# Performance work log

Hardware: AMD Instinct MI355X
Metric: run time of the kernel (lower is better)

## Reference

```python
import jax, jax.numpy as jnp
import numpy as np

N = 50000
E = 800000
D_IN, D_HID, D_OUT = 128, 128, 64


def setup_inputs() -> dict:
    key = jax.random.key(0)
    ks = jax.random.split(key, 8)
    x = jax.random.normal(ks[0], (N, D_IN), dtype=jnp.float32)
    edge_index = jax.random.randint(ks[1], (2, E), 0, N, dtype=jnp.int64)
    # Glorot-ish init for GCNConv linear weights + zero bias (PyG default bias=True)
    def lin(k, din, dout):
        s = 1.0 / np.sqrt(din)
        return jax.random.uniform(k, (din, dout), jnp.float32, -s, s)
    return {
        "x": x,
        "edge_index": edge_index,
        "W1": lin(ks[2], D_IN, D_HID), "b1": jnp.zeros((D_HID,), jnp.float32),
        "W2": lin(ks[3], D_HID, D_HID), "b2": jnp.zeros((D_HID,), jnp.float32),
        "W3": lin(ks[4], D_HID, D_OUT), "b3": jnp.zeros((D_OUT,), jnp.float32),
    }


def _prep_edges(edge_index, n):
    # add self loops (PyG GCNConv default add_self_loops=True)
    loop = jnp.arange(n, dtype=edge_index.dtype)
    src = jnp.concatenate([edge_index[0], loop])
    dst = jnp.concatenate([edge_index[1], loop])
    deg = jax.ops.segment_sum(jnp.ones_like(dst, dtype=jnp.float32), dst, num_segments=n)
    dinv = jnp.where(deg > 0, jax.lax.rsqrt(deg), 0.0)
    norm = dinv[src] * dinv[dst]  # symmetric normalization per edge
    return src, dst, norm


def _gcn_conv(h, W, b, src, dst, norm, n):
    h = h @ W                                   # [N, dout]
    msg = h[src] * norm[:, None]                # [E+N, dout] gather
    out = jax.ops.segment_sum(msg, dst, num_segments=n)  # scatter-add
    return out + b


def reference(x, edge_index, W1, b1, W2, b2, W3, b3):
    src, dst, norm = _prep_edges(edge_index, N)
    h = jax.nn.relu(_gcn_conv(x, W1, b1, src, dst, norm, N))
    h = jax.nn.relu(_gcn_conv(h, W2, b2, src, dst, norm, N))
    return _gcn_conv(h, W3, b3, src, dst, norm, N)  # eval mode: dropout is identity
```

## Files before the change

kernel.cpp:

```cpp
#include <hip/hip_runtime.h>
#include <hip/hip_fp16.h>
#include <math.h>

#define NN 50000
#define NE 800000
#define RAWSTRIDE 96
#define NBUCK 196
#define NBBIN 196
#define BCAP 4608
#define ACH 4096
#define G1B 782

using bf8v = __attribute__((ext_vector_type(8))) short;
using f4v  = __attribute__((ext_vector_type(4))) float;

__device__ inline unsigned short f2bf(float f) {
    unsigned int u = __float_as_uint(f);
    u += 0x7FFFu + ((u >> 16) & 1u);
    return (unsigned short)(u >> 16);
}
__device__ inline float bflo(unsigned int d) { return __uint_as_float(d << 16); }
__device__ inline float bfhi(unsigned int d) { return __uint_as_float(d & 0xFFFF0000u); }


__device__ __forceinline__ void bin_body(const int* __restrict__ src,
                                         const int* __restrict__ dst,
                                         int* __restrict__ gcursor,
                                         unsigned int* __restrict__ bst,
                                         int bx, char* shc) {
    unsigned int* items = (unsigned int*)shc;
    int* cnt    = (int*)(shc + 16384);
    int* pref   = (int*)(shc + 17408);
    int* gstart = (int*)(shc + 18436);
    const int t = threadIdx.x;
    cnt[t] = 0;
    __syncthreads();
    const int base = bx * ACH;

    unsigned int my[16]; int myb[16], myr[16];
    #pragma unroll
    for (int i = 0; i < 16; ++i) {
        int e = base + i * 256 + t;
        my[i] = 0; myb[i] = -1; myr[i] = 0;
        if (e < NE) {
            int d = dst[e], s = src[e];
            my[i] = (unsigned int)s | ((unsigned int)d << 16);
            int b = d >> 8;
            myb[i] = b;
            myr[i] = atomicAdd(&cnt[b], 1);
        }
    }
    __syncthreads();
    if (t == 0) {
        int run = 0;
        for (int b = 0; b < 256; ++b) { pref[b] = run; run += cnt[b]; }
        pref[256] = run;
    }
    __syncthreads();
    if (cnt[t] > 0) gstart[t] = atomicAdd(&gcursor[t], cnt[t]);
    __syncthreads();
    #pragma unroll
    for (int i = 0; i < 16; ++i)
        if (myb[i] >= 0) items[pref[myb[i]] + myr[i]] = my[i];
    __syncthreads();
    const int total = pref[256];
    for (int i = t; i < total; i += 256) {
        int lo = 0, hi = 255;
        while (lo < hi) { int mid = (lo + hi + 1) >> 1; if (pref[mid] <= i) lo = mid; else hi = mid - 1; }
        int idx = gstart[lo] + (i - pref[lo]);
        if (idx < BCAP) bst[(size_t)lo * BCAP + idx] = items[i];
    }
}


__global__ __launch_bounds__(512) void sortb_kernel(const int* __restrict__ gcursor,
                                                    const unsigned int* __restrict__ bst,
                                                    int* __restrict__ cnt_g,
                                                    float* __restrict__ dinv,
                                                    unsigned short* __restrict__ raw) {
    __shared__ unsigned int items[BCAP];
    __shared__ int cnt[256], pref[257], cur[256];
    __shared__ unsigned short outl[BCAP];
    const int b = blockIdx.x;
    const int t = threadIdx.x;
    int n = gcursor[b];
    if (n > BCAP) n = BCAP;
    if (t < 256) { cnt[t] = 0; cur[t] = 0; }
    __syncthreads();
    for (int i = t; i < n; i += 512) {
        unsigned int u = bst[(size_t)b * BCAP + i];
        items[i] = u;
        atomicAdd(&cnt[(u >> 16) & 255], 1);
    }
    __syncthreads();
    if (t == 0) {
        int run = 0;
        for (int j = 0; j < 256; ++j) { pref[j] = run; run += cnt[j]; }
        pref[256] = run;
    }
    __syncthreads();
    for (int i = t; i < n; i += 512) {
        unsigned int u = items[i];
        int ln = (u >> 16) & 255;
        int r = atomicAdd(&cur[ln], 1);
        outl[pref[ln] + r] = (unsigned short)(u & 0xFFFFu);
    }
    __syncthreads();
    for (int i = t; i < n; i += 512) {
        int lo = 0, hi = 255;
        while (lo < hi) { int mid = (lo + hi + 1) >> 1; if (pref[mid] <= i) lo = mid; else hi = mid - 1; }
        int r = i - pref[lo];
        if (r < RAWSTRIDE) raw[(size_t)(b * 256 + lo) * RAWSTRIDE + r] = outl[i];
    }
    if (t < 256) {
        int node = b * 256 + t;
        if (node < NN) {
            int c = cnt[t];
            cnt_g[node] = c;
            dinv[node] = rsqrtf((float)(1 + c));
        }
    }
}


__device__ __forceinline__ void gemm128_body_f32(const float* __restrict__ A,
                                                 const float* __restrict__ W,
                                                 unsigned short* __restrict__ out,
                                                 int bx, char* shc) {
    unsigned short* Wt = (unsigned short*)shc;
    unsigned short* Dt = (unsigned short*)(shc + 128 * 136 * 2);
    const int t = threadIdx.x;
    const int row0 = bx * 64;

    {
        int n = t & 127;
        int kbase = (t >> 7) * 4;
        for (int kk = kbase; kk < 128; kk += 8) {
            float w0 = W[(kk + 0) * 128 + n];
            float w1 = W[(kk + 1) * 128 + n];
            float w2 = W[(kk + 2) * 128 + n];
            float w3 = W[(kk + 3) * 128 + n];
            unsigned int p0 = (unsigned int)f2bf(w0) | ((unsigned int)f2bf(w1) << 16);
            unsigned int p1 = (unsigned int)f2bf(w2) | ((unsigned int)f2bf(w3) << 16);
            *(unsigned int*)&Wt[n * 136 + kk]     = p0;
            *(unsigned int*)&Wt[n * 136 + kk + 2] = p1;
        }
    }
    __syncthreads();

    const int wave = t >> 6;
    const int lane = t & 63;
    const int m16  = lane & 15;
    const int quad = lane >> 4;
    const int arow = row0 + wave * 16 + m16;
    const int arowc = (arow < NN) ? arow : 0;

    f4v acc[8];
    #pragma unroll
    for (int i = 0; i < 8; ++i) acc[i] = (f4v)(0.0f);

    #pragma unroll
    for (int k0 = 0; k0 < 128; k0 += 32) {
        bf8v afrag;
        const float4* ap = (const float4*)(A + (size_t)arowc * 128 + k0 + quad * 8);
        float4 a0 = ap[0], a1 = ap[1];
        afrag[0] = (short)f2bf(a0.x); afrag[1] = (short)f2bf(a0.y);
        afrag[2] = (short)f2bf(a0.z); afrag[3] = (short)f2bf(a0.w);
        afrag[4] = (short)f2bf(a1.x); afrag[5] = (short)f2bf(a1.y);
        afrag[6] = (short)f2bf(a1.z); afrag[7] = (short)f2bf(a1.w);
        #pragma unroll
        for (int nt = 0; nt < 8; ++nt) {
            bf8v bfrag = *(const bf8v*)&Wt[(nt * 16 + m16) * 136 + k0 + quad * 8];
            acc[nt] = __builtin_amdgcn_mfma_f32_16x16x32_bf16(afrag, bfrag, acc[nt], 0, 0, 0);
        }
    }

    #pragma unroll
    for (int nt = 0; nt < 8; ++nt) {
        #pragma unroll
        for (int r = 0; r < 4; ++r) {
            Dt[(wave * 16 + quad * 4 + r) * 136 + nt * 16 + m16] = f2bf(acc[nt][r]);
        }
    }
    __syncthreads();

    {
        int r = t >> 2;
        int c = t & 3;
        int gr = row0 + r;
        if (gr < NN) {
            const uint4* s = (const uint4*)&Dt[r * 136] + c * 4;
            uint4* d = (uint4*)(out + (size_t)gr * 128) + c * 4;
            d[0] = s[0]; d[1] = s[1]; d[2] = s[2]; d[3] = s[3];
        }
    }
}

__global__ __launch_bounds__(256) void bin_g1_kernel(const int* __restrict__ src,
                                                     const int* __restrict__ dst,
                                                     int* __restrict__ gcursor,
                                                     unsigned int* __restrict__ bst,
                                                     const float* __restrict__ x,
                                                     const float* __restrict__ W1,
                                                     unsigned short* __restrict__ hb) {
    __shared__ __align__(16) char sh[52224];
    if (blockIdx.x < NBBIN) {
        bin_body(src, dst, gcursor, bst, blockIdx.x, sh);
    } else {
        gemm128_body_f32(x, W1, hb, blockIdx.x - NBBIN, sh);
    }
}


#define AGG128_BODY(HV, RROW, C, DIW, LANE, ACCV)                                   \
    {                                                                               \
        uint4 g = HV[(size_t)wid * 16 + (LANE)];                                    \
        float ws = (DIW) * (DIW);                                                   \
        ACCV[0] = ws * bflo(g.x); ACCV[1] = ws * bfhi(g.x);                         \
        ACCV[2] = ws * bflo(g.y); ACCV[3] = ws * bfhi(g.y);                         \
        ACCV[4] = ws * bflo(g.z); ACCV[5] = ws * bfhi(g.z);                         \
        ACCV[6] = ws * bflo(g.w); ACCV[7] = ws * bfhi(g.w);                         \
    }                                                                               \
    const int cfull = (C) & ~7;                                                     \
    uint4 q;                                                                        \
    if (cfull > 0) q = *(const uint4*)(RROW);                                       \
    for (int e = 0; e < cfull; e += 8) {                                            \
        uint4 qc = q;                                                               \
        if (e + 8 < cfull) q = *(const uint4*)((RROW) + e + 8);                     \
        int c0 = qc.x & 0xFFFFu, c1 = qc.x >> 16;                                   \
        int c2 = qc.y & 0xFFFFu, c3 = qc.y >> 16;                                   \
        int c4 = qc.z & 0xFFFFu, c5 = qc.z >> 16;                                   \
        int c6 = qc.w & 0xFFFFu, c7 = qc.w >> 16;                                   \
        uint4 g0 = HV[(size_t)c0 * 16 + (LANE)];                                    \
        uint4 g1 = HV[(size_t)c1 * 16 + (LANE)];                                    \
        uint4 g2 = HV[(size_t)c2 * 16 + (LANE)];                                    \
        uint4 g3 = HV[(size_t)c3 * 16 + (LANE)];                                    \
        uint4 g4 = HV[(size_t)c4 * 16 + (LANE)];                                    \
        uint4 g5 = HV[(size_t)c5 * 16 + (LANE)];                                    \
        uint4 g6 = HV[(size_t)c6 * 16 + (LANE)];                                    \
        uint4 g7 = HV[(size_t)c7 * 16 + (LANE)];                                    \
        float w0 = (DIW) * dinv[c0], w1 = (DIW) * dinv[c1];                         \
        float w2 = (DIW) * dinv[c2], w3 = (DIW) * dinv[c3];                         \
        float w4 = (DIW) * dinv[c4], w5 = (DIW) * dinv[c5];                         \
        float w6 = (DIW) * dinv[c6], w7 = (DIW) * dinv[c7];                         \
        ACC8(g0, w0) ACC8(g1, w1) ACC8(g2, w2) ACC8(g3, w3)                         \
        ACC8(g4, w4) ACC8(g5, w5) ACC8(g6, w6) ACC8(g7, w7)                         \
    }                                                                               \
    if ((C) & 7) {                                                                  \
        int e = cfull, rem = (C) - e;                                               \
        uint4 qc = *(const uint4*)((RROW) + e);                                     \
        int c0 = qc.x & 0xFFFFu, c1 = qc.x >> 16;                                   \
        int c2 = qc.y & 0xFFFFu, c3 = qc.y >> 16;                                   \
        int c4 = qc.z & 0xFFFFu, c5 = qc.z >> 16;                                   \
        int c6 = qc.w & 0xFFFFu, c7 = qc.w >> 16;                                   \
        if (rem <= 1) c1 = 0; if (rem <= 2) c2 = 0; if (rem <= 3) c3 = 0;           \
        if (rem <= 4) c4 = 0; if (rem <= 5) c5 = 0; if (rem <= 6) c6 = 0;           \
        c7 = 0;                                                                     \
        float w0 = (DIW) * dinv[c0];                                                \
        float w1 = (rem > 1) ? (DIW) * dinv[c1] : 0.f;                              \
        float w2 = (rem > 2) ? (DIW) * dinv[c2] : 0.f;                              \
        float w3 = (rem > 3) ? (DIW) * dinv[c3] : 0.f;                              \
        float w4 = (rem > 4) ? (DIW) * dinv[c4] : 0.f;                              \
        float w5 = (rem > 5) ? (DIW) * dinv[c5] : 0.f;                              \
        float w6 = (rem > 6) ? (DIW) * dinv[c6] : 0.f;                              \
        float w7 = 0.f;                                                             \
        uint4 g0 = HV[(size_t)c0 * 16 + (LANE)];                                    \
        uint4 g1 = HV[(size_t)c1 * 16 + (LANE)];                                    \
        uint4 g2 = HV[(size_t)c2 * 16 + (LANE)];                                    \
        uint4 g3 = HV[(size_t)c3 * 16 + (LANE)];                                    \
        uint4 g4 = HV[(size_t)c4 * 16 + (LANE)];                                    \
        uint4 g5 = HV[(size_t)c5 * 16 + (LANE)];                                    \
        uint4 g6 = HV[(size_t)c6 * 16 + (LANE)];                                    \
        uint4 g7 = HV[(size_t)c7 * 16 + (LANE)];                                    \
        ACC8(g0, w0) ACC8(g1, w1) ACC8(g2, w2) ACC8(g3, w3)                         \
        ACC8(g4, w4) ACC8(g5, w5) ACC8(g6, w6) ACC8(g7, w7)                         \
    }

#define ACC8(G, W_) \
    acc[0] += W_ * bflo(G.x); acc[1] += W_ * bfhi(G.x); \
    acc[2] += W_ * bflo(G.y); acc[3] += W_ * bfhi(G.y); \
    acc[4] += W_ * bflo(G.z); acc[5] += W_ * bfhi(G.z); \
    acc[6] += W_ * bflo(G.w); acc[7] += W_ * bfhi(G.w);


__global__ __launch_bounds__(256) void aggW2_kernel(const unsigned short* __restrict__ hin,
                                                    const unsigned short* __restrict__ raw,
                                                    const int* __restrict__ cnt_g,
                                                    const float* __restrict__ dinv,
                                                    const float* __restrict__ bias,
                                                    const float* __restrict__ W,
                                                    unsigned short* __restrict__ out) {
    __shared__ unsigned short Wt[128 * 136];
    __shared__ unsigned short Zt[64 * 136];
    const int t = threadIdx.x;
    const int row0 = blockIdx.x * 64;

    {
        int n = t & 127;
        int kbase = (t >> 7) * 4;
        for (int kk = kbase; kk < 128; kk += 8) {
            float w0 = W[(kk + 0) * 128 + n];
            float w1 = W[(kk + 1) * 128 + n];
            float w2 = W[(kk + 2) * 128 + n];
            float w3 = W[(kk + 3) * 128 + n];
            unsigned int p0 = (unsigned int)f2bf(w0) | ((unsigned int)f2bf(w1) << 16);
            unsigned int p1 = (unsigned int)f2bf(w2) | ((unsigned int)f2bf(w3) << 16);
            *(unsigned int*)&Wt[n * 136 + kk]     = p0;
            *(unsigned int*)&Wt[n * 136 + kk + 2] = p1;
        }
    }

    const int group = t >> 4;
    const int lane  = t & 15;
    const uint4* hv = (const uint4*)hin;
    const float4* bp = (const float4*)bias;
    float4 b0 = bp[lane * 2], b1 = bp[lane * 2 + 1];

    for (int r = 0; r < 4; ++r) {
        const int wid = row0 + r * 16 + group;
        uint4 o = make_uint4(0u, 0u, 0u, 0u);
        if (wid < NN) {
            int c = cnt_g[wid];
            if (c > RAWSTRIDE) c = RAWSTRIDE;
            const float diw = dinv[wid];
            const unsigned short* rrow = raw + (size_t)wid * RAWSTRIDE;
            float acc[8];
            AGG128_BODY(hv, rrow, c, diw, lane, acc)
            acc[0] += b0.x; acc[1] += b0.y; acc[2] += b0.z; acc[3] += b0.w;
            acc[4] += b1.x; acc[5] += b1.y; acc[6] += b1.z; acc[7] += b1.w;
            #pragma unroll
            for (int j = 0; j < 8; ++j) acc[j] = fmaxf(acc[j], 0.f);
            o.x = (unsigned int)f2bf(acc[0]) | ((unsigned int)f2bf(acc[1]) << 16);
            o.y = (unsigned int)f2bf(acc[2]) | ((unsigned int)f2bf(acc[3]) << 16);
            o.z = (unsigned int)f2bf(acc[4]) | ((unsigned int)f2bf(acc[5]) << 16);
            o.w = (unsigned int)f2bf(acc[6]) | ((unsigned int)f2bf(acc[7]) << 16);
        }
        *(uint4*)&Zt[(r * 16 + group) * 136 + lane * 8] = o;
    }
    __syncthreads();

    const int wave = t >> 6;
    const int l64  = t & 63;
    const int m16  = l64 & 15;
    const int quad = l64 >> 4;

    f4v acc[8];
    #pragma unroll
    for (int i = 0; i < 8; ++i) acc[i] = (f4v)(0.0f);

    #pragma unroll
    for (int k0 = 0; k0 < 128; k0 += 32) {
        bf8v afrag = *(const bf8v*)&Zt[(wave * 16 + m16) * 136 + k0 + quad * 8];
        #pragma unroll
        for (int nt = 0; nt < 8; ++nt) {
            bf8v bfrag = *(const bf8v*)&Wt[(nt * 16 + m16) * 136 + k0 + quad * 8];
            acc[nt] = __builtin_amdgcn_mfma_f32_16x16x32_bf16(afrag, bfrag, acc[nt], 0, 0, 0);
        }
    }
    __syncthreads();

    #pragma unroll
    for (int nt = 0; nt < 8; ++nt) {
        #pragma unroll
        for (int r = 0; r < 4; ++r) {
            Zt[(wave * 16 + quad * 4 + r) * 136 + nt * 16 + m16] = f2bf(acc[nt][r]);
        }
    }
    __syncthreads();

    {
        int r = t >> 2;
        int c = t & 3;
        int gr = row0 + r;
        if (gr < NN) {
            const uint4* s = (const uint4*)&Zt[r * 136] + c * 4;
            uint4* d = (uint4*)(out + (size_t)gr * 128) + c * 4;
            d[0] = s[0]; d[1] = s[1]; d[2] = s[2]; d[3] = s[3];
        }
    }
}


__global__ __launch_bounds__(256) void aggG3_kernel(const unsigned short* __restrict__ hin,
                                                    const unsigned short* __restrict__ raw,
                                                    const int* __restrict__ cnt_g,
                                                    const float* __restrict__ dinv,
                                                    const float* __restrict__ bias,
                                                    const float* __restrict__ W,
                                                    unsigned short* __restrict__ outh) {
    constexpr int LD = 132;
    __shared__ float Zt[64 * LD];
    const int t = threadIdx.x;
    const int row0 = blockIdx.x * 64;

    const int group = t >> 4;
    const int lane  = t & 15;
    const uint4* hv = (const uint4*)hin;
    const float4* bp = (const float4*)bias;
    float4 b0 = bp[lane * 2], b1 = bp[lane * 2 + 1];

    for (int r = 0; r < 4; ++r) {
        const int wid = row0 + r * 16 + group;
        float acc[8] = {0.f, 0.f, 0.f, 0.f, 0.f, 0.f, 0.f, 0.f};
        if (wid < NN) {
            int c = cnt_g[wid];
            if (c > RAWSTRIDE) c = RAWSTRIDE;
            const float diw = dinv[wid];
            const unsigned short* rrow = raw + (size_t)wid * RAWSTRIDE;
            AGG128_BODY(hv, rrow, c, diw, lane, acc)
            acc[0] += b0.x; acc[1] += b0.y; acc[2] += b0.z; acc[3] += b0.w;
            acc[4] += b1.x; acc[5] += b1.y; acc[6] += b1.z; acc[7] += b1.w;
            #pragma unroll
            for (int j = 0; j < 8; ++j) acc[j] = fmaxf(acc[j], 0.f);
        }
        float4* zr = (float4*)&Zt[(r * 16 + group) * LD + lane * 8];
        zr[0] = make_float4(acc[0], acc[1], acc[2], acc[3]);
        zr[1] = make_float4(acc[4], acc[5], acc[6], acc[7]);
    }
    __syncthreads();

    constexpr int CG = 16;
    constexpr int RPT = 4;
    const int cg = t % CG;
    const int rt = t / CG;
    const float4* Wv = (const float4*)W;
    float4 acc[RPT];
    #pragma unroll
    for (int i = 0; i < RPT; ++i) acc[i] = make_float4(0.f, 0.f, 0.f, 0.f);

    for (int k0 = 0; k0 < 128; k0 += 4) {
        float4 w0 = Wv[(k0 + 0) * CG + cg];
        float4 w1 = Wv[(k0 + 1) * CG + cg];
        float4 w2 = Wv[(k0 + 2) * CG + cg];
        float4 w3 = Wv[(k0 + 3) * CG + cg];
        #pragma unroll
        for (int i = 0; i < RPT; ++i) {
            const float* lr = Zt + (rt * RPT + i) * LD;
            float4 a = ((const float4*)lr)[k0 >> 2];
            acc[i].x += a.x * w0.x + a.y * w1.x + a.z * w2.x + a.w * w3.x;
            acc[i].y += a.x * w0.y + a.y * w1.y + a.z * w2.y + a.w * w3.y;
            acc[i].z += a.x * w0.z + a.y * w1.z + a.z * w2.z + a.w * w3.z;
            acc[i].w += a.x * w0.w + a.y * w1.w + a.z * w2.w + a.w * w3.w;
        }
    }

    #pragma unroll
    for (int i = 0; i < RPT; ++i) {
        int gr = row0 + rt * RPT + i;
        if (gr < NN) {
            uint2 o;
            o.x = (unsigned int)f2bf(acc[i].x) | ((unsigned int)f2bf(acc[i].y) << 16);
            o.y = (unsigned int)f2bf(acc[i].z) | ((unsigned int)f2bf(acc[i].w) << 16);
            ((uint2*)(outh + (size_t)gr * 64))[cg] = o;
        }
    }
}


__global__ __launch_bounds__(256) void agg3_kernel(const unsigned short* __restrict__ hin,
                                                   const unsigned short* __restrict__ raw,
                                                   const int* __restrict__ cnt_g,
                                                   const float* __restrict__ dinv,
                                                   const float* __restrict__ bias,
                                                   float* __restrict__ out) {
    const int t = threadIdx.x;
    const int group = t >> 3;
    const int lane  = t & 7;
    const int wid = blockIdx.x * 32 + group;
    if (wid >= NN) return;

    int c = cnt_g[wid];
    if (c > RAWSTRIDE) c = RAWSTRIDE;
    const float diw = dinv[wid];
    const unsigned short* rrow = raw + (size_t)wid * RAWSTRIDE;
    const uint4* hv = (const uint4*)hin;

    float acc[8];
    {
        uint4 g = hv[(size_t)wid * 8 + lane];
        float ws = diw * diw;
        acc[0] = ws * bflo(g.x); acc[1] = ws * bfhi(g.x);
        acc[2] = ws * bflo(g.y); acc[3] = ws * bfhi(g.y);
        acc[4] = ws * bflo(g.z); acc[5] = ws * bfhi(g.z);
        acc[6] = ws * bflo(g.w); acc[7] = ws * bfhi(g.w);
    }

    const int cfull = c & ~7;
    uint4 q;
    if (cfull > 0) q = *(const uint4*)(rrow);
    for (int e = 0; e < cfull; e += 8) {
        uint4 qc = q;
        if (e + 8 < cfull) q = *(const uint4*)(rrow + e + 8);
        int c0 = qc.x & 0xFFFFu, c1 = qc.x >> 16;
        int c2 = qc.y & 0xFFFFu, c3 = qc.y >> 16;
        int c4 = qc.z & 0xFFFFu, c5 = qc.z >> 16;
        int c6 = qc.w & 0xFFFFu, c7 = qc.w >> 16;
        uint4 g0 = hv[(size_t)c0 * 8 + lane];
        uint4 g1 = hv[(size_t)c1 * 8 + lane];
        uint4 g2 = hv[(size_t)c2 * 8 + lane];
        uint4 g3 = hv[(size_t)c3 * 8 + lane];
        uint4 g4 = hv[(size_t)c4 * 8 + lane];
        uint4 g5 = hv[(size_t)c5 * 8 + lane];
        uint4 g6 = hv[(size_t)c6 * 8 + lane];
        uint4 g7 = hv[(size_t)c7 * 8 + lane];
        float w0 = diw * dinv[c0], w1 = diw * dinv[c1];
        float w2 = diw * dinv[c2], w3 = diw * dinv[c3];
        float w4 = diw * dinv[c4], w5 = diw * dinv[c5];
        float w6 = diw * dinv[c6], w7 = diw * dinv[c7];
        ACC8(g0, w0) ACC8(g1, w1) ACC8(g2, w2) ACC8(g3, w3)
        ACC8(g4, w4) ACC8(g5, w5) ACC8(g6, w6) ACC8(g7, w7)
    }
    if (c & 7) {
        int e = cfull, rem = c - e;
        uint4 qc = *(const uint4*)(rrow + e);
        int c0 = qc.x & 0xFFFFu, c1 = qc.x >> 16;
        int c2 = qc.y & 0xFFFFu, c3 = qc.y >> 16;
        int c4 = qc.z & 0xFFFFu, c5 = qc.z >> 16;
        int c6 = qc.w & 0xFFFFu, c7 = qc.w >> 16;
        if (rem <= 1) c1 = 0; if (rem <= 2) c2 = 0; if (rem <= 3) c3 = 0;
        if (rem <= 4) c4 = 0; if (rem <= 5) c5 = 0; if (rem <= 6) c6 = 0;
        c7 = 0;
        float w0 = diw * dinv[c0];
        float w1 = (rem > 1) ? diw * dinv[c1] : 0.f;
        float w2 = (rem > 2) ? diw * dinv[c2] : 0.f;
        float w3 = (rem > 3) ? diw * dinv[c3] : 0.f;
        float w4 = (rem > 4) ? diw * dinv[c4] : 0.f;
        float w5 = (rem > 5) ? diw * dinv[c5] : 0.f;
        float w6 = (rem > 6) ? diw * dinv[c6] : 0.f;
        float w7 = 0.f;
        uint4 g0 = hv[(size_t)c0 * 8 + lane];
        uint4 g1 = hv[(size_t)c1 * 8 + lane];
        uint4 g2 = hv[(size_t)c2 * 8 + lane];
        uint4 g3 = hv[(size_t)c3 * 8 + lane];
        uint4 g4 = hv[(size_t)c4 * 8 + lane];
        uint4 g5 = hv[(size_t)c5 * 8 + lane];
        uint4 g6 = hv[(size_t)c6 * 8 + lane];
        uint4 g7 = hv[(size_t)c7 * 8 + lane];
        ACC8(g0, w0) ACC8(g1, w1) ACC8(g2, w2) ACC8(g3, w3)
        ACC8(g4, w4) ACC8(g5, w5) ACC8(g6, w6) ACC8(g7, w7)
    }

    const float4* bp = (const float4*)bias;
    float4 b0 = bp[lane * 2], b1 = bp[lane * 2 + 1];
    acc[0] += b0.x; acc[1] += b0.y; acc[2] += b0.z; acc[3] += b0.w;
    acc[4] += b1.x; acc[5] += b1.y; acc[6] += b1.z; acc[7] += b1.w;

    float4 o0 = make_float4(acc[0], acc[1], acc[2], acc[3]);
    float4 o1 = make_float4(acc[4], acc[5], acc[6], acc[7]);
    ((float4*)(out + (size_t)wid * 64))[lane * 2]     = o0;
    ((float4*)(out + (size_t)wid * 64))[lane * 2 + 1] = o1;
}


extern "C" void kernel_launch(void* const* d_in, const int* in_sizes, int n_in,
                              void* d_out, int out_size, void* d_ws, size_t ws_size,
                              hipStream_t stream) {
    const float* x  = (const float*)d_in[0];
    const int*   ei = (const int*)d_in[1];
    const float* W1 = (const float*)d_in[2];
    const float* b1 = (const float*)d_in[3];
    const float* W2 = (const float*)d_in[4];
    const float* b2 = (const float*)d_in[5];
    const float* W3 = (const float*)d_in[6];
    const float* b3 = (const float*)d_in[7];
    float* out = (float*)d_out;

    char* w = (char*)d_ws;
    int*   cnt_g   = (int*)  (w + 0x0000000);
    int*   gcursor = (int*)  (w + 0x0040000);
    float* dinv    = (float*)(w + 0x0048000);
    unsigned int*   bst = (unsigned int*)  (w + 0x0080000);
    unsigned short* raw = (unsigned short*)(w + 0x0400000);
    unsigned short* hb  = (unsigned short*)(w + 0x0E00000);
    unsigned short* h2b = (unsigned short*)(w + 0x1B00000);
    unsigned short* h3b = (unsigned short*)(w + 0x2800000);

    const int* src = ei;
    const int* dst = ei + NE;

    hipMemsetAsync(gcursor, 0, NBUCK * sizeof(int), stream);
    bin_g1_kernel<<<NBBIN + G1B, 256, 0, stream>>>(src, dst, gcursor, bst, x, W1, hb);
    sortb_kernel<<<NBUCK, 512, 0, stream>>>(gcursor, bst, cnt_g, dinv, raw);
    aggW2_kernel<<<G1B, 256, 0, stream>>>(hb, raw, cnt_g, dinv, b1, W2, h2b);
    aggG3_kernel<<<G1B, 256, 0, stream>>>(h2b, raw, cnt_g, dinv, b2, W3, h3b);
    agg3_kernel<<<(NN + 31) / 32, 256, 0, stream>>>(h3b, raw, cnt_g, dinv, b3, out);
}
```

Before: 239.4 us.

## Pre-convert weights to bf16 once and halve rows per aggregation block

A new prep kernel converts W1 and W2 to transposed bf16 in global memory once, and also zeroes the bucket cursors, which replaces the memset. The GEMM stages now read B fragments straight from global or L2 instead of staging a 128x136 weight tile in LDS in every block. Shared memory shrinks sharply and the aggregation kernels process 32 rows per block over twice as many blocks. Both changes aim at higher occupancy and removing redundant per-block weight conversion. aggG3 also stores its intermediate in bf16 LDS rather than fp32, trading extra global weight reads and added precision loss for less LDS.

```diff
diff --git a/kernel.cpp b/kernel.cpp
--- a/kernel.cpp
+++ b/kernel.cpp
@@ -10,6 +10,7 @@
 #define BCAP 4608
 #define ACH 4096
 #define G1B 782
+#define G2B 1563
 
 using bf8v = __attribute__((ext_vector_type(8))) short;
 using f4v  = __attribute__((ext_vector_type(4))) float;
@@ -21,6 +22,26 @@
 }
 __device__ inline float bflo(unsigned int d) { return __uint_as_float(d << 16); }
 __device__ inline float bfhi(unsigned int d) { return __uint_as_float(d & 0xFFFF0000u); }
+
+
+__global__ __launch_bounds__(256) void prep_kernel(const float* __restrict__ W1,
+                                                   const float* __restrict__ W2,
+                                                   unsigned int* __restrict__ w1p,
+                                                   unsigned int* __restrict__ w2p,
+                                                   int* __restrict__ gcursor) {
+    int id = blockIdx.x * 256 + threadIdx.x;
+    int m = id >> 13;
+    int rest = id & 8191;
+    int n = rest >> 6;
+    int kp = rest & 63;
+    int k = kp * 2;
+    const float* W = m ? W2 : W1;
+    unsigned int* o = m ? w2p : w1p;
+    unsigned int p = (unsigned int)f2bf(W[k * 128 + n]) |
+                     ((unsigned int)f2bf(W[(k + 1) * 128 + n]) << 16);
+    o[n * 64 + kp] = p;
+    if (id < NBUCK) gcursor[id] = 0;
+}
 
 
 __device__ __forceinline__ void bin_body(const int* __restrict__ src,
@@ -124,34 +145,16 @@
 
 
 __device__ __forceinline__ void gemm128_body_f32(const float* __restrict__ A,
-                                                 const float* __restrict__ W,
+                                                 const unsigned short* __restrict__ Wbf,
                                                  unsigned short* __restrict__ out,
                                                  int bx, char* shc) {
-    unsigned short* Wt = (unsigned short*)shc;
-    unsigned short* Dt = (unsigned short*)(shc + 128 * 136 * 2);
+    unsigned short* Dt = (unsigned short*)shc;
     const int t = threadIdx.x;
     const int row0 = bx * 64;
-
-    {
-        int n = t & 127;
-        int kbase = (t >> 7) * 4;
-        for (int kk = kbase; kk < 128; kk += 8) {
-            float w0 = W[(kk + 0) * 128 + n];
-            float w1 = W[(kk + 1) * 128 + n];
-            float w2 = W[(kk + 2) * 128 + n];
-            float w3 = W[(kk + 3) * 128 + n];
-            unsigned int p0 = (unsigned int)f2bf(w0) | ((unsigned int)f2bf(w1) << 16);
-            unsigned int p1 = (unsigned int)f2bf(w2) | ((unsigned int)f2bf(w3) << 16);
-            *(unsigned int*)&Wt[n * 136 + kk]     = p0;
-            *(unsigned int*)&Wt[n * 136 + kk + 2] = p1;
-        }
-    }
-    __syncthreads();
-
     const int wave = t >> 6;
-    const int lane = t & 63;
-    const int m16  = lane & 15;
-    const int quad = lane >> 4;
+    const int l64  = t & 63;
+    const int m16  = l64 & 15;
+    const int quad = l64 >> 4;
     const int arow = row0 + wave * 16 + m16;
     const int arowc = (arow < NN) ? arow : 0;
 
@@ -170,7 +173,7 @@
         afrag[6] = (short)f2bf(a1.z); afrag[7] = (short)f2bf(a1.w);
         #pragma unroll
         for (int nt = 0; nt < 8; ++nt) {
-            bf8v bfrag = *(const bf8v*)&Wt[(nt * 16 + m16) * 136 + k0 + quad * 8];
+            bf8v bfrag = *(const bf8v*)(Wbf + (nt * 16 + m16) * 128 + k0 + quad * 8);
             acc[nt] = __builtin_amdgcn_mfma_f32_16x16x32_bf16(afrag, bfrag, acc[nt], 0, 0, 0);
         }
     }
@@ -184,15 +187,13 @@
     }
     __syncthreads();
 
-    {
-        int r = t >> 2;
-        int c = t & 3;
+    #pragma unroll
+    for (int j = 0; j < 4; ++j) {
+        int idx = j * 256 + t;
+        int r = idx >> 4, c4 = idx & 15;
         int gr = row0 + r;
-        if (gr < NN) {
-            const uint4* s = (const uint4*)&Dt[r * 136] + c * 4;
-            uint4* d = (uint4*)(out + (size_t)gr * 128) + c * 4;
-            d[0] = s[0]; d[1] = s[1]; d[2] = s[2]; d[3] = s[3];
-        }
+        if (gr < NN)
+            ((uint4*)(out + (size_t)gr * 128))[c4] = ((const uint4*)&Dt[r * 136])[c4];
     }
 }
 
@@ -201,25 +202,31 @@
                                                      int* __restrict__ gcursor,
                                                      unsigned int* __restrict__ bst,
                                                      const float* __restrict__ x,
-                                                     const float* __restrict__ W1,
+                                                     const unsigned short* __restrict__ w1bf,
                                                      unsigned short* __restrict__ hb) {
-    __shared__ __align__(16) char sh[52224];
+    __shared__ __align__(16) char sh[19472];
     if (blockIdx.x < NBBIN) {
         bin_body(src, dst, gcursor, bst, blockIdx.x, sh);
     } else {
-        gemm128_body_f32(x, W1, hb, blockIdx.x - NBBIN, sh);
-    }
-}
-
-
-#define AGG128_BODY(HV, RROW, C, DIW, LANE, ACCV)                                   \
+        gemm128_body_f32(x, w1bf, hb, blockIdx.x - NBBIN, sh);
+    }
+}
+
+
+#define ACC8(G, W_) \
+    acc[0] += W_ * bflo(G.x); acc[1] += W_ * bfhi(G.x); \
+    acc[2] += W_ * bflo(G.y); acc[3] += W_ * bfhi(G.y); \
+    acc[4] += W_ * bflo(G.z); acc[5] += W_ * bfhi(G.z); \
+    acc[6] += W_ * bflo(G.w); acc[7] += W_ * bfhi(G.w);
+
+#define AGG128_BODY(HV, RROW, C, DIW, LANE)                                         \
     {                                                                               \
         uint4 g = HV[(size_t)wid * 16 + (LANE)];                                    \
         float ws = (DIW) * (DIW);                                                   \
-        ACCV[0] = ws * bflo(g.x); ACCV[1] = ws * bfhi(g.x);                         \
-        ACCV[2] = ws * bflo(g.y); ACCV[3] = ws * bfhi(g.y);                         \
-        ACCV[4] = ws * bflo(g.z); ACCV[5] = ws * bfhi(g.z);                         \
-        ACCV[6] = ws * bflo(g.w); ACCV[7] = ws * bfhi(g.w);                         \
+        acc[0] = ws * bflo(g.x); acc[1] = ws * bfhi(g.x);                           \
+        acc[2] = ws * bflo(g.y); acc[3] = ws * bfhi(g.y);                           \
+        acc[4] = ws * bflo(g.z); acc[5] = ws * bfhi(g.z);                           \
+        acc[6] = ws * bflo(g.w); acc[7] = ws * bfhi(g.w);                           \
     }                                                                               \
     const int cfull = (C) & ~7;                                                     \
     uint4 q;                                                                        \
@@ -276,47 +283,24 @@
         ACC8(g4, w4) ACC8(g5, w5) ACC8(g6, w6) ACC8(g7, w7)                         \
     }
 
-#define ACC8(G, W_) \
-    acc[0] += W_ * bflo(G.x); acc[1] += W_ * bfhi(G.x); \
-    acc[2] += W_ * bflo(G.y); acc[3] += W_ * bfhi(G.y); \
-    acc[4] += W_ * bflo(G.z); acc[5] += W_ * bfhi(G.z); \
-    acc[6] += W_ * bflo(G.w); acc[7] += W_ * bfhi(G.w);
-
 
 __global__ __launch_bounds__(256) void aggW2_kernel(const unsigned short* __restrict__ hin,
                                                     const unsigned short* __restrict__ raw,
                                                     const int* __restrict__ cnt_g,
                                                     const float* __restrict__ dinv,
                                                     const float* __restrict__ bias,
-                                                    const float* __restrict__ W,
+                                                    const unsigned short* __restrict__ Wbf,
                                                     unsigned short* __restrict__ out) {
-    __shared__ unsigned short Wt[128 * 136];
-    __shared__ unsigned short Zt[64 * 136];
+    __shared__ unsigned short Zt[32 * 136];
     const int t = threadIdx.x;
-    const int row0 = blockIdx.x * 64;
-
-    {
-        int n = t & 127;
-        int kbase = (t >> 7) * 4;
-        for (int kk = kbase; kk < 128; kk += 8) {
-            float w0 = W[(kk + 0) * 128 + n];
-            float w1 = W[(kk + 1) * 128 + n];
-            float w2 = W[(kk + 2) * 128 + n];
-            float w3 = W[(kk + 3) * 128 + n];
-            unsigned int p0 = (unsigned int)f2bf(w0) | ((unsigned int)f2bf(w1) << 16);
-            unsigned int p1 = (unsigned int)f2bf(w2) | ((unsigned int)f2bf(w3) << 16);
-            *(unsigned int*)&Wt[n * 136 + kk]     = p0;
-            *(unsigned int*)&Wt[n * 136 + kk + 2] = p1;
-        }
-    }
-
+    const int row0 = blockIdx.x * 32;
     const int group = t >> 4;
     const int lane  = t & 15;
     const uint4* hv = (const uint4*)hin;
     const float4* bp = (const float4*)bias;
-    float4 b0 = bp[lane * 2], b1 = bp[lane * 2 + 1];
-
-    for (int r = 0; r < 4; ++r) {
+    float4 bv0 = bp[lane * 2], bv1 = bp[lane * 2 + 1];
+
+    for (int r = 0; r < 2; ++r) {
         const int wid = row0 + r * 16 + group;
         uint4 o = make_uint4(0u, 0u, 0u, 0u);
         if (wid < NN) {
@@ -325,9 +309,9 @@
             const float diw = dinv[wid];
             const unsigned short* rrow = raw + (size_t)wid * RAWSTRIDE;
             float acc[8];
-            AGG128_BODY(hv, rrow, c, diw, lane, acc)
-            acc[0] += b0.x; acc[1] += b0.y; acc[2] += b0.z; acc[3] += b0.w;
-            acc[4] += b1.x; acc[5] += b1.y; acc[6] += b1.z; acc[7] += b1.w;
+            AGG128_BODY(hv, rrow, c, diw, lane)
+            acc[0] += bv0.x; acc[1] += bv0.y; acc[2] += bv0.z; acc[3] += bv0.w;
+            acc[4] += bv1.x; acc[5] += bv1.y; acc[6] += bv1.z; acc[7] += bv1.w;
             #pragma unroll
             for (int j = 0; j < 8; ++j) acc[j] = fmaxf(acc[j], 0.f);
             o.x = (unsigned int)f2bf(acc[0]) | ((unsigned int)f2bf(acc[1]) << 16);
@@ -343,40 +327,41 @@
     const int l64  = t & 63;
     const int m16  = l64 & 15;
     const int quad = l64 >> 4;
-
-    f4v acc[8];
-    #pragma unroll
-    for (int i = 0; i < 8; ++i) acc[i] = (f4v)(0.0f);
+    const int rh = wave & 1;
+    const int nh = wave >> 1;
+
+    f4v acc[4];
+    #pragma unroll
+    for (int i = 0; i < 4; ++i) acc[i] = (f4v)(0.0f);
 
     #pragma unroll
     for (int k0 = 0; k0 < 128; k0 += 32) {
-        bf8v afrag = *(const bf8v*)&Zt[(wave * 16 + m16) * 136 + k0 + quad * 8];
+        bf8v afrag = *(const bf8v*)&Zt[(rh * 16 + m16) * 136 + k0 + quad * 8];
         #pragma unroll
-        for (int nt = 0; nt < 8; ++nt) {
-            bf8v bfrag = *(const bf8v*)&Wt[(nt * 16 + m16) * 136 + k0 + quad * 8];
-            acc[nt] = __builtin_amdgcn_mfma_f32_16x16x32_bf16(afrag, bfrag, acc[nt], 0, 0, 0);
-        }
-    }
-    __syncthreads();
-
-    #pragma unroll
-    for (int nt = 0; nt < 8; ++nt) {
+        for (int j = 0; j < 4; ++j) {
+            int nt = nh * 4 + j;
+            bf8v bfrag = *(const bf8v*)(Wbf + (nt * 16 + m16) * 128 + k0 + quad * 8);
+            acc[j] = __builtin_amdgcn_mfma_f32_16x16x32_bf16(afrag, bfrag, acc[j], 0, 0, 0);
+        }
+    }
+    __syncthreads();
+
+    #pragma unroll
+    for (int j = 0; j < 4; ++j) {
         #pragma unroll
-        for (int r = 0; r < 4; ++r) {
-            Zt[(wave * 16 + quad * 4 + r) * 136 + nt * 16 + m16] = f2bf(acc[nt][r]);
-        }
-    }
-    __syncthreads();
-
-    {
-        int r = t >> 2;
-        int c = t & 3;
+        for (int rr = 0; rr < 4; ++rr) {
+            Zt[(rh * 16 + quad * 4 + rr) * 136 + (nh * 4 + j) * 16 + m16] = f2bf(acc[j][rr]);
+        }
+    }
+    __syncthreads();
+
+    #pragma unroll
+    for (int jj = 0; jj < 2; ++jj) {
+        int idx = jj * 256 + t;
+        int r = idx >> 4, c4 = idx & 15;
         int gr = row0 + r;
-        if (gr < NN) {
-            const uint4* s = (const uint4*)&Zt[r * 136] + c * 4;
-            uint4* d = (uint4*)(out + (size_t)gr * 128) + c * 4;
-            d[0] = s[0]; d[1] = s[1]; d[2] = s[2]; d[3] = s[3];
-        }
+        if (gr < NN)
+            ((uint4*)(out + (size_t)gr * 128))[c4] = ((const uint4*)&Zt[r * 136])[c4];
     }
 }
 
@@ -388,65 +373,64 @@
                                                     const float* __restrict__ bias,
                                                     const float* __restrict__ W,
                                                     unsigned short* __restrict__ outh) {
-    constexpr int LD = 132;
-    __shared__ float Zt[64 * LD];
+    __shared__ unsigned short Zt[32 * 136];
     const int t = threadIdx.x;
-    const int row0 = blockIdx.x * 64;
-
+    const int row0 = blockIdx.x * 32;
     const int group = t >> 4;
     const int lane  = t & 15;
     const uint4* hv = (const uint4*)hin;
     const float4* bp = (const float4*)bias;
-    float4 b0 = bp[lane * 2], b1 = bp[lane * 2 + 1];
-
-    for (int r = 0; r < 4; ++r) {
+    float4 bv0 = bp[lane * 2], bv1 = bp[lane * 2 + 1];
+
+    for (int r = 0; r < 2; ++r) {
         const int wid = row0 + r * 16 + group;
-        float acc[8] = {0.f, 0.f, 0.f, 0.f, 0.f, 0.f, 0.f, 0.f};
+        uint4 o = make_uint4(0u, 0u, 0u, 0u);
         if (wid < NN) {
             int c = cnt_g[wid];
             if (c > RAWSTRIDE) c = RAWSTRIDE;
             const float diw = dinv[wid];
             const unsigned short* rrow = raw + (size_t)wid * RAWSTRIDE;
-            AGG128_BODY(hv, rrow, c, diw, lane, acc)
-            acc[0] += b0.x; acc[1] += b0.y; acc[2] += b0.z; acc[3] += b0.w;
-            acc[4] += b1.x; acc[5] += b1.y; acc[6] += b1.z; acc[7] += b1.w;
+            float acc[8];
+            AGG128_BODY(hv, rrow, c, diw, lane)
+            acc[0] += bv0.x; acc[1] += bv0.y; acc[2] += bv0.z; acc[3] += bv0.w;
+            acc[4] += bv1.x; acc[5] += bv1.y; acc[6] += bv1.z; acc[7] += bv1.w;
             #pragma unroll
             for (int j = 0; j < 8; ++j) acc[j] = fmaxf(acc[j], 0.f);
-        }
-        float4* zr = (float4*)&Zt[(r * 16 + group) * LD + lane * 8];
-        zr[0] = make_float4(acc[0], acc[1], acc[2], acc[3]);
-        zr[1] = make_float4(acc[4], acc[5], acc[6], acc[7]);
-    }
-    __syncthreads();
-
-    constexpr int CG = 16;
-    constexpr int RPT = 4;
-    const int cg = t % CG;
-    const int rt = t / CG;
+            o.x = (unsigned int)f2bf(acc[0]) | ((unsigned int)f2bf(acc[1]) << 16);
+            o.y = (unsigned int)f2bf(acc[2]) | ((unsigned int)f2bf(acc[3]) << 16);
+            o.z = (unsigned int)f2bf(acc[4]) | ((unsigned int)f2bf(acc[5]) << 16);
+            o.w = (unsigned int)f2bf(acc[6]) | ((unsigned int)f2bf(acc[7]) << 16);
+        }
+        *(uint4*)&Zt[(r * 16 + group) * 136 + lane * 8] = o;
+    }
+    __syncthreads();
+
+    const int cg = t & 15;
+    const int rt = t >> 4;
     const float4* Wv = (const float4*)W;
-    float4 acc[RPT];
-    #pragma unroll
-    for (int i = 0; i < RPT; ++i) acc[i] = make_float4(0.f, 0.f, 0.f, 0.f);
+    float4 acc[2];
+    acc[0] = make_float4(0.f, 0.f, 0.f, 0.f);
+    acc[1] = make_float4(0.f, 0.f, 0.f, 0.f);
 
     for (int k0 = 0; k0 < 128; k0 += 4) {
-        float4 w0 = Wv[(k0 + 0) * CG + cg];
-        float4 w1 = Wv[(k0 + 1) * CG + cg];
-        float4 w2 = Wv[(k0 + 2) * CG + cg];
-        float4 w3 = Wv[(k0 + 3) * CG + cg];
+        float4 w0 = Wv[(k0 + 0) * 16 + cg];
+        float4 w1 = Wv[(k0 + 1) * 16 + cg];
+        float4 w2 = Wv[(k0 + 2) * 16 + cg];
+        float4 w3 = Wv[(k0 + 3) * 16 + cg];
         #pragma unroll
-        for (int i = 0; i < RPT; ++i) {
-            const float* lr = Zt + (rt * RPT + i) * LD;
-            float4 a = ((const float4*)lr)[k0 >> 2];
-            acc[i].x += a.x * w0.x + a.y * w1.x + a.z * w2.x + a.w * w3.x;
-            acc[i].y += a.x * w0.y + a.y * w1.y + a.z * w2.y + a.w * w3.y;
-            acc[i].z += a.x * w0.z + a.y * w1.z + a.z * w2.z + a.w * w3.z;
-            acc[i].w += a.x * w0.w + a.y * w1.w + a.z * w2.w + a.w * w3.w;
-        }
-    }
-
-    #pragma unroll
-    for (int i = 0; i < RPT; ++i) {
-        int gr = row0 + rt * RPT + i;
+        for (int i = 0; i < 2; ++i) {
+            uint2 u = *(const uint2*)&Zt[(rt * 2 + i) * 136 + k0];
+            float ax = bflo(u.x), ay = bfhi(u.x), az = bflo(u.y), aw = bfhi(u.y);
+            acc[i].x += ax * w0.x + ay * w1.x + az * w2.x + aw * w3.x;
+            acc[i].y += ax * w0.y + ay * w1.y + az * w2.y + aw * w3.y;
+            acc[i].z += ax * w0.z + ay * w1.z + az * w2.z + aw * w3.z;
+            acc[i].w += ax * w0.w + ay * w1.w + az * w2.w + aw * w3.w;
+        }
+    }
+
+    #pragma unroll
+    for (int i = 0; i < 2; ++i) {
+        int gr = row0 + rt * 2 + i;
         if (gr < NN) {
             uint2 o;
             o.x = (unsigned int)f2bf(acc[i].x) | ((unsigned int)f2bf(acc[i].y) << 16);
@@ -569,8 +553,10 @@
     int*   cnt_g   = (int*)  (w + 0x0000000);
     int*   gcursor = (int*)  (w + 0x0040000);
     float* dinv    = (float*)(w + 0x0048000);
-    unsigned int*   bst = (unsigned int*)  (w + 0x0080000);
-    unsigned short* raw = (unsigned short*)(w + 0x0400000);
+    unsigned int*   w1p = (unsigned int*)  (w + 0x0080000);
+    unsigned int*   w2p = (unsigned int*)  (w + 0x0088000);
+    unsigned int*   bst = (unsigned int*)  (w + 0x0090000);
+    unsigned short* raw = (unsigned short*)(w + 0x0480000);
     unsigned short* hb  = (unsigned short*)(w + 0x0E00000);
     unsigned short* h2b = (unsigned short*)(w + 0x1B00000);
     unsigned short* h3b = (unsigned short*)(w + 0x2800000);
@@ -578,10 +564,12 @@
     const int* src = ei;
     const int* dst = ei + NE;
 
-    hipMemsetAsync(gcursor, 0, NBUCK * sizeof(int), stream);
-    bin_g1_kernel<<<NBBIN + G1B, 256, 0, stream>>>(src, dst, gcursor, bst, x, W1, hb);
+    prep_kernel<<<64, 256, 0, stream>>>(W1, W2, w1p, w2p, gcursor);
+    bin_g1_kernel<<<NBBIN + G1B, 256, 0, stream>>>(src, dst, gcursor, bst, x,
+                                                   (const unsigned short*)w1p, hb);
     sortb_kernel<<<NBUCK, 512, 0, stream>>>(gcursor, bst, cnt_g, dinv, raw);
-    aggW2_kernel<<<G1B, 256, 0, stream>>>(hb, raw, cnt_g, dinv, b1, W2, h2b);
-    aggG3_kernel<<<G1B, 256, 0, stream>>>(h2b, raw, cnt_g, dinv, b2, W3, h3b);
+    aggW2_kernel<<<G2B, 256, 0, stream>>>(hb, raw, cnt_g, dinv, b1,
+                                          (const unsigned short*)w2p, h2b);
+    aggG3_kernel<<<G2B, 256, 0, stream>>>(h2b, raw, cnt_g, dinv, b2, W3, h3b);
     agg3_kernel<<<(NN + 31) / 32, 256, 0, stream>>>(h3b, raw, cnt_g, dinv, b3, out);
 }
```

Result: slower. 245.0 us (+2.4%).

## Split fused aggregate+GEMM kernels into standalone aggregation and GEMM kernels

Applied to the files above, without the earlier changes.

Splits the fused aggregate-then-transform kernels for layers 2 and 3 into a standalone gather/aggregate kernel (16 rows per block, 3125 blocks) and separate GEMM kernels that read the aggregated bf16 rows from a workspace buffer. The aim is higher occupancy and better latency hiding for the irregular gather, since it no longer shares a block and LDS with the GEMM. The cost is an extra round trip of an N×128 bf16 intermediate through global memory and two extra kernel launches per forward.

```diff
diff --git a/kernel.cpp b/kernel.cpp
--- a/kernel.cpp
+++ b/kernel.cpp
@@ -10,6 +10,7 @@
 #define BCAP 4608
 #define ACH 4096
 #define G1B 782
+#define GAB 3125
 
 using bf8v = __attribute__((ext_vector_type(8))) short;
 using f4v  = __attribute__((ext_vector_type(4))) float;
@@ -212,14 +213,20 @@
 }
 
 
-#define AGG128_BODY(HV, RROW, C, DIW, LANE, ACCV)                                   \
+#define ACC8(G, W_) \
+    acc[0] += W_ * bflo(G.x); acc[1] += W_ * bfhi(G.x); \
+    acc[2] += W_ * bflo(G.y); acc[3] += W_ * bfhi(G.y); \
+    acc[4] += W_ * bflo(G.z); acc[5] += W_ * bfhi(G.z); \
+    acc[6] += W_ * bflo(G.w); acc[7] += W_ * bfhi(G.w);
+
+#define AGG128_BODY(HV, RROW, C, DIW, LANE)                                         \
     {                                                                               \
         uint4 g = HV[(size_t)wid * 16 + (LANE)];                                    \
         float ws = (DIW) * (DIW);                                                   \
-        ACCV[0] = ws * bflo(g.x); ACCV[1] = ws * bfhi(g.x);                         \
-        ACCV[2] = ws * bflo(g.y); ACCV[3] = ws * bfhi(g.y);                         \
-        ACCV[4] = ws * bflo(g.z); ACCV[5] = ws * bfhi(g.z);                         \
-        ACCV[6] = ws * bflo(g.w); ACCV[7] = ws * bfhi(g.w);                         \
+        acc[0] = ws * bflo(g.x); acc[1] = ws * bfhi(g.x);                           \
+        acc[2] = ws * bflo(g.y); acc[3] = ws * bfhi(g.y);                           \
+        acc[4] = ws * bflo(g.z); acc[5] = ws * bfhi(g.z);                           \
+        acc[6] = ws * bflo(g.w); acc[7] = ws * bfhi(g.w);                           \
     }                                                                               \
     const int cfull = (C) & ~7;                                                     \
     uint4 q;                                                                        \
@@ -276,18 +283,47 @@
         ACC8(g4, w4) ACC8(g5, w5) ACC8(g6, w6) ACC8(g7, w7)                         \
     }
 
-#define ACC8(G, W_) \
-    acc[0] += W_ * bflo(G.x); acc[1] += W_ * bfhi(G.x); \
-    acc[2] += W_ * bflo(G.y); acc[3] += W_ * bfhi(G.y); \
-    acc[4] += W_ * bflo(G.z); acc[5] += W_ * bfhi(G.z); \
-    acc[6] += W_ * bflo(G.w); acc[7] += W_ * bfhi(G.w);
-
-
-__global__ __launch_bounds__(256) void aggW2_kernel(const unsigned short* __restrict__ hin,
-                                                    const unsigned short* __restrict__ raw,
-                                                    const int* __restrict__ cnt_g,
-                                                    const float* __restrict__ dinv,
-                                                    const float* __restrict__ bias,
+
+template <bool RELU>
+__global__ __launch_bounds__(256) void agg128_sa_kernel(const unsigned short* __restrict__ hin,
+                                                        const unsigned short* __restrict__ raw,
+                                                        const int* __restrict__ cnt_g,
+                                                        const float* __restrict__ dinv,
+                                                        const float* __restrict__ bias,
+                                                        unsigned short* __restrict__ outb) {
+    const int t = threadIdx.x;
+    const int group = t >> 4;
+    const int lane  = t & 15;
+    const int wid = blockIdx.x * 16 + group;
+    if (wid >= NN) return;
+
+    int c = cnt_g[wid];
+    if (c > RAWSTRIDE) c = RAWSTRIDE;
+    const float diw = dinv[wid];
+    const unsigned short* rrow = raw + (size_t)wid * RAWSTRIDE;
+    const uint4* hv = (const uint4*)hin;
+
+    float acc[8];
+    AGG128_BODY(hv, rrow, c, diw, lane)
+
+    const float4* bp = (const float4*)bias;
+    float4 b0 = bp[lane * 2], b1 = bp[lane * 2 + 1];
+    acc[0] += b0.x; acc[1] += b0.y; acc[2] += b0.z; acc[3] += b0.w;
+    acc[4] += b1.x; acc[5] += b1.y; acc[6] += b1.z; acc[7] += b1.w;
+    if (RELU) {
+        #pragma unroll
+        for (int j = 0; j < 8; ++j) acc[j] = fmaxf(acc[j], 0.f);
+    }
+    uint4 o;
+    o.x = (unsigned int)f2bf(acc[0]) | ((unsigned int)f2bf(acc[1]) << 16);
+    o.y = (unsigned int)f2bf(acc[2]) | ((unsigned int)f2bf(acc[3]) << 16);
+    o.z = (unsigned int)f2bf(acc[4]) | ((unsigned int)f2bf(acc[5]) << 16);
+    o.w = (unsigned int)f2bf(acc[6]) | ((unsigned int)f2bf(acc[7]) << 16);
+    ((uint4*)(outb + (size_t)wid * 128))[lane] = o;
+}
+
+
+__global__ __launch_bounds__(256) void gemm2_kernel(const unsigned short* __restrict__ z1,
                                                     const float* __restrict__ W,
                                                     unsigned short* __restrict__ out) {
     __shared__ unsigned short Wt[128 * 136];
@@ -309,33 +345,14 @@
             *(unsigned int*)&Wt[n * 136 + kk + 2] = p1;
         }
     }
-
-    const int group = t >> 4;
-    const int lane  = t & 15;
-    const uint4* hv = (const uint4*)hin;
-    const float4* bp = (const float4*)bias;
-    float4 b0 = bp[lane * 2], b1 = bp[lane * 2 + 1];
-
-    for (int r = 0; r < 4; ++r) {
-        const int wid = row0 + r * 16 + group;
-        uint4 o = make_uint4(0u, 0u, 0u, 0u);
-        if (wid < NN) {
-            int c = cnt_g[wid];
-            if (c > RAWSTRIDE) c = RAWSTRIDE;
-            const float diw = dinv[wid];
-            const unsigned short* rrow = raw + (size_t)wid * RAWSTRIDE;
-            float acc[8];
-            AGG128_BODY(hv, rrow, c, diw, lane, acc)
-            acc[0] += b0.x; acc[1] += b0.y; acc[2] += b0.z; acc[3] += b0.w;
-            acc[4] += b1.x; acc[5] += b1.y; acc[6] += b1.z; acc[7] += b1.w;
-            #pragma unroll
-            for (int j = 0; j < 8; ++j) acc[j] = fmaxf(acc[j], 0.f);
-            o.x = (unsigned int)f2bf(acc[0]) | ((unsigned int)f2bf(acc[1]) << 16);
-            o.y = (unsigned int)f2bf(acc[2]) | ((unsigned int)f2bf(acc[3]) << 16);
-            o.z = (unsigned int)f2bf(acc[4]) | ((unsigned int)f2bf(acc[5]) << 16);
-            o.w = (unsigned int)f2bf(acc[6]) | ((unsigned int)f2bf(acc[7]) << 16);
-        }
-        *(uint4*)&Zt[(r * 16 + group) * 136 + lane * 8] = o;
+    #pragma unroll
+    for (int j = 0; j < 4; ++j) {
+        int idx = j * 256 + t;
+        int r = idx >> 4, c4 = idx & 15;
+        int gr = row0 + r;
+        uint4 v = make_uint4(0u, 0u, 0u, 0u);
+        if (gr < NN) v = ((const uint4*)(z1 + (size_t)gr * 128))[c4];
+        *(uint4*)&Zt[r * 136 + c4 * 8] = v;
     }
     __syncthreads();
 
@@ -381,46 +398,30 @@
 }
 
 
-__global__ __launch_bounds__(256) void aggG3_kernel(const unsigned short* __restrict__ hin,
-                                                    const unsigned short* __restrict__ raw,
-                                                    const int* __restrict__ cnt_g,
-                                                    const float* __restrict__ dinv,
-                                                    const float* __restrict__ bias,
+__global__ __launch_bounds__(256) void gemm3_kernel(const unsigned short* __restrict__ Ab,
                                                     const float* __restrict__ W,
                                                     unsigned short* __restrict__ outh) {
-    constexpr int LD = 132;
-    __shared__ float Zt[64 * LD];
-    const int t = threadIdx.x;
-    const int row0 = blockIdx.x * 64;
-
-    const int group = t >> 4;
-    const int lane  = t & 15;
-    const uint4* hv = (const uint4*)hin;
-    const float4* bp = (const float4*)bias;
-    float4 b0 = bp[lane * 2], b1 = bp[lane * 2 + 1];
-
-    for (int r = 0; r < 4; ++r) {
-        const int wid = row0 + r * 16 + group;
-        float acc[8] = {0.f, 0.f, 0.f, 0.f, 0.f, 0.f, 0.f, 0.f};
-        if (wid < NN) {
-            int c = cnt_g[wid];
-            if (c > RAWSTRIDE) c = RAWSTRIDE;
-            const float diw = dinv[wid];
-            const unsigned short* rrow = raw + (size_t)wid * RAWSTRIDE;
-            AGG128_BODY(hv, rrow, c, diw, lane, acc)
-            acc[0] += b0.x; acc[1] += b0.y; acc[2] += b0.z; acc[3] += b0.w;
-            acc[4] += b1.x; acc[5] += b1.y; acc[6] += b1.z; acc[7] += b1.w;
-            #pragma unroll
-            for (int j = 0; j < 8; ++j) acc[j] = fmaxf(acc[j], 0.f);
-        }
-        float4* zr = (float4*)&Zt[(r * 16 + group) * LD + lane * 8];
-        zr[0] = make_float4(acc[0], acc[1], acc[2], acc[3]);
-        zr[1] = make_float4(acc[4], acc[5], acc[6], acc[7]);
-    }
-    __syncthreads();
-
     constexpr int CG = 16;
     constexpr int RPT = 4;
+    constexpr int ROWS = 64;
+    constexpr int LD = 132;
+    __shared__ float lds[ROWS * LD];
+    const int t = threadIdx.x;
+    const int row0 = blockIdx.x * ROWS;
+
+    #pragma unroll
+    for (int j = 0; j < ROWS / 8; ++j) {
+        int idx4 = j * 256 + t;
+        int r = idx4 >> 5, c4 = idx4 & 31;
+        int gr = row0 + r;
+        uint2 u = make_uint2(0u, 0u);
+        if (gr < NN) u = ((const uint2*)(Ab + (size_t)gr * 128))[c4];
+        float4 v;
+        v.x = bflo(u.x); v.y = bfhi(u.x); v.z = bflo(u.y); v.w = bfhi(u.y);
+        ((float4*)(lds + r * LD))[c4] = v;
+    }
+    __syncthreads();
+
     const int cg = t % CG;
     const int rt = t / CG;
     const float4* Wv = (const float4*)W;
@@ -435,7 +436,7 @@
         float4 w3 = Wv[(k0 + 3) * CG + cg];
         #pragma unroll
         for (int i = 0; i < RPT; ++i) {
-            const float* lr = Zt + (rt * RPT + i) * LD;
+            const float* lr = lds + (rt * RPT + i) * LD;
             float4 a = ((const float4*)lr)[k0 >> 2];
             acc[i].x += a.x * w0.x + a.y * w1.x + a.z * w2.x + a.w * w3.x;
             acc[i].y += a.x * w0.y + a.y * w1.y + a.z * w2.y + a.w * w3.y;
@@ -572,7 +573,7 @@
     unsigned int*   bst = (unsigned int*)  (w + 0x0080000);
     unsigned short* raw = (unsigned short*)(w + 0x0400000);
     unsigned short* hb  = (unsigned short*)(w + 0x0E00000);
-    unsigned short* h2b = (unsigned short*)(w + 0x1B00000);
+    unsigned short* zb  = (unsigned short*)(w + 0x1B00000);
     unsigned short* h3b = (unsigned short*)(w + 0x2800000);
 
     const int* src = ei;
@@ -581,7 +582,9 @@
     hipMemsetAsync(gcursor, 0, NBUCK * sizeof(int), stream);
     bin_g1_kernel<<<NBBIN + G1B, 256, 0, stream>>>(src, dst, gcursor, bst, x, W1, hb);
     sortb_kernel<<<NBUCK, 512, 0, stream>>>(gcursor, bst, cnt_g, dinv, raw);
-    aggW2_kernel<<<G1B, 256, 0, stream>>>(hb, raw, cnt_g, dinv, b1, W2, h2b);
-    aggG3_kernel<<<G1B, 256, 0, stream>>>(h2b, raw, cnt_g, dinv, b2, W3, h3b);
+    agg128_sa_kernel<true><<<GAB, 256, 0, stream>>>(hb, raw, cnt_g, dinv, b1, zb);
+    gemm2_kernel<<<G1B, 256, 0, stream>>>(zb, W2, hb);
+    agg128_sa_kernel<true><<<GAB, 256, 0, stream>>>(hb, raw, cnt_g, dinv, b2, zb);
+    gemm3_kernel<<<G1B, 256, 0, stream>>>(zb, W3, h3b);
     agg3_kernel<<<(NN + 31) / 32, 256, 0, stream>>>(h3b, raw, cnt_g, dinv, b3, out);
 }
```

Result: slower. 247.2 us (+3.3%).
